# Performance work log

Hardware: AMD Instinct MI355X
Metric: run time of the kernel (lower is better)

## Reference

```python
import jax, jax.numpy as jnp
import numpy as np

N = 50000
E = 800000
NFEAT, NHID, NCLASS = 128, 128, 40


def setup_inputs() -> dict:
    key = jax.random.key(0)
    ks = jax.random.split(key, 8)
    x = jax.random.normal(ks[0], (N, NFEAT), dtype=jnp.float32)
    edge_index = jax.random.randint(ks[1], (2, E), 0, N, dtype=jnp.int64)
    def glorot(k, fan_in, fan_out):
        s = jnp.sqrt(6.0 / (fan_in + fan_out)).astype(jnp.float32)
        return jax.random.uniform(k, (fan_in, fan_out), jnp.float32, -s, s)
    W1 = glorot(ks[2], NFEAT, NHID); b1 = jnp.zeros((NHID,), jnp.float32)
    W2 = glorot(ks[3], NHID, NHID);  b2 = jnp.zeros((NHID,), jnp.float32)
    W3 = glorot(ks[4], NHID, NCLASS); b3 = jnp.zeros((NCLASS,), jnp.float32)
    return {"x": x, "edge_index": edge_index,
            "W1": W1, "b1": b1, "W2": W2, "b2": b2, "W3": W3, "b3": b3}


def _gcn_norm(edge_index, num_nodes, dtype):
    # Add self-loops, then symmetric normalization D^-1/2 (A+I) D^-1/2 (PyG gcn_norm).
    loop = jnp.arange(num_nodes, dtype=edge_index.dtype)
    src = jnp.concatenate([edge_index[0], loop])
    dst = jnp.concatenate([edge_index[1], loop])
    deg = jax.ops.segment_sum(jnp.ones_like(src, dtype=dtype), dst, num_segments=num_nodes)
    dinv = jnp.where(deg > 0, deg ** -0.5, 0.0).astype(dtype)
    norm = dinv[src] * dinv[dst]  # [E+N]
    return src, dst, norm


def _gcn_conv(h, src, dst, norm, W, b, num_nodes):
    h = h @ W                              # dense transform first (out_dim small)
    msg = h[src] * norm[:, None]           # gather + per-edge scale
    out = jax.ops.segment_sum(msg, dst, num_segments=num_nodes)  # scatter-add
    return out + b


def reference(x, edge_index, W1, b1, W2, b2, W3, b3):
    src, dst, norm = _gcn_norm(edge_index, N, x.dtype)
    h = jax.nn.relu(_gcn_conv(x, src, dst, norm, W1, b1, N))  # dropout: eval mode (identity)
    h = jax.nn.relu(_gcn_conv(h, src, dst, norm, W2, b2, N))
    h = _gcn_conv(h, src, dst, norm, W3, b3, N)
    return jax.nn.log_softmax(h, axis=-1)
```

## Files before the change

### kernel.cpp

```cpp
#include <hip/hip_runtime.h>
#include <stdint.h>

#define NN 50000
#define NE 800000
#define GG 782
#define NB 196
#define TT 8192
#define TB 98

typedef __attribute__((ext_vector_type(8))) short bfx8;
typedef __attribute__((ext_vector_type(4))) float f32x4;

__device__ inline unsigned short f2bf(float f) {
    union { float f; uint32_t u; } x; x.f = f;
    uint32_t u = x.u;
    return (unsigned short)((u + 0x7fffu + ((u >> 16) & 1u)) >> 16);
}
__device__ inline uint32_t pack2bf(float lo, float hi) {
    return (uint32_t)f2bf(lo) | ((uint32_t)f2bf(hi) << 16);
}
__device__ inline float bf2f(unsigned short h) {
    union { uint32_t u; float f; } c; c.u = ((uint32_t)h) << 16;
    return c.f;
}
__device__ inline float2 bfp2f2(uint32_t v) {
    union { uint32_t u; float f; } a, b;
    a.u = (v & 0xffffu) << 16;
    b.u = v & 0xffff0000u;
    return make_float2(a.f, b.f);
}
__device__ inline bfx8 ld8(const unsigned short* p) {
    union { uint4 u; bfx8 v; } c;
    c.u = *(const uint4*)p;
    return c.v;
}
__device__ inline bfx8 cvt8(float4 u, float4 v) {
    union { unsigned short s[8]; bfx8 r; } c;
    c.s[0] = f2bf(u.x); c.s[1] = f2bf(u.y); c.s[2] = f2bf(u.z); c.s[3] = f2bf(u.w);
    c.s[4] = f2bf(v.x); c.s[5] = f2bf(v.y); c.s[6] = f2bf(v.z); c.s[7] = f2bf(v.w);
    return c.r;
}

__global__ void prep(const float* __restrict__ W1, const float* __restrict__ W2,
                     const float* __restrict__ W3,
                     unsigned short* __restrict__ WT1, unsigned short* __restrict__ WT2,
                     unsigned short* __restrict__ WT3) {
    int w = blockIdx.x * 256 + threadIdx.x;
    if (w < 16384) {
        int nn = w >> 7, k = w & 127;
        WT1[nn * 128 + k] = f2bf(W1[k * 128 + nn]);
    } else if (w < 32768) {
        int w2 = w - 16384, nn = w2 >> 7, k = w2 & 127;
        WT2[nn * 128 + k] = f2bf(W2[k * 128 + nn]);
    } else if (w < 38912) {
        int w2 = w - 32768, nn = w2 >> 7, k = w2 & 127;
        WT3[nn * 128 + k] = (nn < 40) ? f2bf(W3[k * 40 + nn]) : (unsigned short)0;
    }
}

__global__ __launch_bounds__(256) void gemm1_hist(const float* __restrict__ X,
                                                  const unsigned short* __restrict__ WT,
                                                  unsigned short* __restrict__ G, int n,
                                                  const int* __restrict__ dst,
                                                  int* __restrict__ counts, int e) {
    if (blockIdx.x >= GG) {
        int b = blockIdx.x - GG;
        __shared__ int h[256];
        h[threadIdx.x] = 0;
        __syncthreads();
        int start = b * TT;
        int end = start + TT; if (end > e) end = e;
        for (int i = start + threadIdx.x; i < end; i += 256)
            atomicAdd(&h[dst[i] >> 8], 1);
        __syncthreads();
        int d = threadIdx.x;
        if (d < NB) counts[d * TB + b] = h[d];
        return;
    }
    int wave = threadIdx.x >> 6;
    int lane = threadIdx.x & 63;
    int quad = lane >> 4;
    int c = lane & 15;
    int rowbase = blockIdx.x * 64 + wave * 16;

    int arow = rowbase + c;
    if (arow >= n) arow = n - 1;
    const float* ap = X + (size_t)arow * 128 + quad * 8;
    bfx8 a[4];
#pragma unroll
    for (int kc = 0; kc < 4; kc++) {
        float4 u = *(const float4*)(ap + kc * 32);
        float4 v = *(const float4*)(ap + kc * 32 + 4);
        a[kc] = cvt8(u, v);
    }

    f32x4 acc[8];
#pragma unroll
    for (int ct = 0; ct < 8; ct++) acc[ct] = (f32x4){0.f, 0.f, 0.f, 0.f};
#pragma unroll
    for (int ct = 0; ct < 8; ct++) {
        const unsigned short* bp = WT + (size_t)(ct * 16 + c) * 128 + quad * 8;
#pragma unroll
        for (int kc = 0; kc < 4; kc++) {
            bfx8 b = ld8(bp + kc * 32);
            acc[ct] = __builtin_amdgcn_mfma_f32_16x16x32_bf16(a[kc], b, acc[ct], 0, 0, 0);
        }
    }

    int r0 = rowbase + quad * 4;
    bool odd = lane & 1;
#pragma unroll
    for (int ct = 0; ct < 8; ct++) {
        float x0 = acc[ct][0], x1 = acc[ct][1], x2 = acc[ct][2], x3 = acc[ct][3];
        float y0 = __shfl_xor(x0, 1, 64), y1 = __shfl_xor(x1, 1, 64);
        float y2 = __shfl_xor(x2, 1, 64), y3 = __shfl_xor(x3, 1, 64);
        int colp = ct * 16 + (c & ~1);
        if (!odd) {
            if (r0 + 0 < n) *(uint32_t*)(&G[(size_t)(r0 + 0) * 128 + colp]) = pack2bf(x0, y0);
            if (r0 + 1 < n) *(uint32_t*)(&G[(size_t)(r0 + 1) * 128 + colp]) = pack2bf(x1, y1);
        } else {
            if (r0 + 2 < n) *(uint32_t*)(&G[(size_t)(r0 + 2) * 128 + colp]) = pack2bf(y2, x2);
            if (r0 + 3 < n) *(uint32_t*)(&G[(size_t)(r0 + 3) * 128 + colp]) = pack2bf(y3, x3);
        }
    }
}

__global__ void scanA(int* __restrict__ counts, int* __restrict__ base196) {
    __shared__ int s[256];
    int d = threadIdx.x;
    int run = 0;
    if (d < NB) {
        for (int b0 = 0; b0 < TB; b0 += 14) {
            int c[14];
#pragma unroll
            for (int j = 0; j < 14; j++) {
                int b = b0 + j;
                c[j] = (b < TB) ? counts[d * TB + b] : 0;
            }
#pragma unroll
            for (int j = 0; j < 14; j++) {
                int b = b0 + j;
                if (b < TB) counts[d * TB + b] = run;
                run += c[j];
            }
        }
    }
    int v = run;
    s[d] = v;
    __syncthreads();
#pragma unroll
    for (int off = 1; off < 256; off <<= 1) {
        int y = (d >= off) ? s[d - off] : 0;
        __syncthreads();
        s[d] += y;
        __syncthreads();
    }
    if (d <= NB) base196[d] = s[d] - v;
}

__global__ __launch_bounds__(256) void scatterA(const int* __restrict__ src,
                                                const int* __restrict__ dst,
                                                const int* __restrict__ counts,
                                                const int* __restrict__ base196,
                                                uint32_t* __restrict__ packA, int e) {
    __shared__ int gb[256];
    __shared__ int lc[256];
    int t = threadIdx.x;
    if (t < NB) {
        gb[t] = base196[t] + counts[t * TB + blockIdx.x];
        lc[t] = 0;
    }
    __syncthreads();
    int start = blockIdx.x * TT;
    int end = start + TT; if (end > e) end = e;
    for (int i = start + t; i < end; i += 256) {
        int d = dst[i];
        int s = src[i];
        int hi = d >> 8;
        int r = atomicAdd(&lc[hi], 1);
        packA[gb[hi] + r] = ((uint32_t)d << 16) | (uint32_t)s;
    }
}

__global__ __launch_bounds__(256) void buildB(const uint32_t* __restrict__ packA,
                                              const int* __restrict__ base196,
                                              int* __restrict__ row_ptr, int* __restrict__ deg,
                                              float* __restrict__ dinv,
                                              unsigned short* __restrict__ csr_src, int n) {
    __shared__ int cnt[256];
    __shared__ int s[256];
    __shared__ int rp[256];
    int hi = blockIdx.x;
    int t = threadIdx.x;
    cnt[t] = 0;
    __syncthreads();
    int b0 = base196[hi], b1 = base196[hi + 1];
    for (int i = b0 + t; i < b1; i += 256)
        atomicAdd(&cnt[(packA[i] >> 16) & 0xFF], 1);
    __syncthreads();
    int v = cnt[t];
    s[t] = v;
    __syncthreads();
#pragma unroll
    for (int off = 1; off < 256; off <<= 1) {
        int y = (t >= off) ? s[t - off] : 0;
        __syncthreads();
        s[t] += y;
        __syncthreads();
    }
    rp[t] = b0 + s[t] - v;
    int node = hi * 256 + t;
    if (node < n) {
        row_ptr[node] = rp[t];
        deg[node] = v;
        dinv[node] = rsqrtf(1.0f + (float)v);
    }
    cnt[t] = 0;
    __syncthreads();
    for (int i = b0 + t; i < b1; i += 256) {
        uint32_t p = packA[i];
        int lo = (p >> 16) & 0xFF;
        int r = atomicAdd(&cnt[lo], 1);
        csr_src[rp[lo] + r] = (unsigned short)(p & 0xFFFF);
    }
}

__global__ __launch_bounds__(256) void gemm128_mfma(const unsigned short* __restrict__ A,
                                                    const unsigned short* __restrict__ WT,
                                                    const float* __restrict__ dinv,
                                                    unsigned short* __restrict__ G, int n) {
    int wave = threadIdx.x >> 6;
    int lane = threadIdx.x & 63;
    int quad = lane >> 4;
    int c = lane & 15;
    int rowbase = blockIdx.x * 64 + wave * 16;

    int arow = rowbase + c;
    if (arow >= n) arow = n - 1;
    const unsigned short* ap = A + (size_t)arow * 128 + quad * 8;
    bfx8 a[4];
#pragma unroll
    for (int kc = 0; kc < 4; kc++) a[kc] = ld8(ap + kc * 32);

    f32x4 acc[8];
#pragma unroll
    for (int ct = 0; ct < 8; ct++) acc[ct] = (f32x4){0.f, 0.f, 0.f, 0.f};
#pragma unroll
    for (int ct = 0; ct < 8; ct++) {
        const unsigned short* bp = WT + (size_t)(ct * 16 + c) * 128 + quad * 8;
#pragma unroll
        for (int kc = 0; kc < 4; kc++) {
            bfx8 b = ld8(bp + kc * 32);
            acc[ct] = __builtin_amdgcn_mfma_f32_16x16x32_bf16(a[kc], b, acc[ct], 0, 0, 0);
        }
    }

    int r0 = rowbase + quad * 4;
    float di[4];
#pragma unroll
    for (int r = 0; r < 4; r++) {
        int rr = r0 + r;
        di[r] = dinv[rr < n ? rr : 0];
    }
    bool odd = lane & 1;
#pragma unroll
    for (int ct = 0; ct < 8; ct++) {
        float x0 = acc[ct][0], x1 = acc[ct][1], x2 = acc[ct][2], x3 = acc[ct][3];
        float y0 = __shfl_xor(x0, 1, 64), y1 = __shfl_xor(x1, 1, 64);
        float y2 = __shfl_xor(x2, 1, 64), y3 = __shfl_xor(x3, 1, 64);
        int colp = ct * 16 + (c & ~1);
        if (!odd) {
            if (r0 + 0 < n) *(uint32_t*)(&G[(size_t)(r0 + 0) * 128 + colp]) = pack2bf(di[0] * x0, di[0] * y0);
            if (r0 + 1 < n) *(uint32_t*)(&G[(size_t)(r0 + 1) * 128 + colp]) = pack2bf(di[1] * x1, di[1] * y1);
        } else {
            if (r0 + 2 < n) *(uint32_t*)(&G[(size_t)(r0 + 2) * 128 + colp]) = pack2bf(di[2] * y2, di[2] * x2);
            if (r0 + 3 < n) *(uint32_t*)(&G[(size_t)(r0 + 3) * 128 + colp]) = pack2bf(di[3] * y3, di[3] * x3);
        }
    }
}

__global__ __launch_bounds__(256) void gemm40_mfma(const unsigned short* __restrict__ A,
                                                   const unsigned short* __restrict__ WT,
                                                   const float* __restrict__ dinv,
                                                   unsigned short* __restrict__ G, int n) {
    int wave = threadIdx.x >> 6;
    int lane = threadIdx.x & 63;
    int quad = lane >> 4;
    int c = lane & 15;
    int rowbase = blockIdx.x * 64 + wave * 16;

    int arow = rowbase + c;
    if (arow >= n) arow = n - 1;
    const unsigned short* ap = A + (size_t)arow * 128 + quad * 8;
    bfx8 a[4];
#pragma unroll
    for (int kc = 0; kc < 4; kc++) a[kc] = ld8(ap + kc * 32);

    f32x4 acc[3];
#pragma unroll
    for (int ct = 0; ct < 3; ct++) acc[ct] = (f32x4){0.f, 0.f, 0.f, 0.f};
#pragma unroll
    for (int ct = 0; ct < 3; ct++) {
        const unsigned short* bp = WT + (size_t)(ct * 16 + c) * 128 + quad * 8;
#pragma unroll
        for (int kc = 0; kc < 4; kc++) {
            bfx8 b = ld8(bp + kc * 32);
            acc[ct] = __builtin_amdgcn_mfma_f32_16x16x32_bf16(a[kc], b, acc[ct], 0, 0, 0);
        }
    }

    int r0 = rowbase + quad * 4;
    float di[4];
#pragma unroll
    for (int r = 0; r < 4; r++) {
        int rr = r0 + r;
        di[r] = dinv[rr < n ? rr : 0];
    }
    bool odd = lane & 1;
#pragma unroll
    for (int ct = 0; ct < 3; ct++) {
        float x0 = acc[ct][0], x1 = acc[ct][1], x2 = acc[ct][2], x3 = acc[ct][3];
        float y0 = __shfl_xor(x0, 1, 64), y1 = __shfl_xor(x1, 1, 64);
        float y2 = __shfl_xor(x2, 1, 64), y3 = __shfl_xor(x3, 1, 64);
        int colp = ct * 16 + (c & ~1);
        if (colp >= 40) continue;
        if (!odd) {
            if (r0 + 0 < n) *(uint32_t*)(&G[(size_t)(r0 + 0) * 40 + colp]) = pack2bf(di[0] * x0, di[0] * y0);
            if (r0 + 1 < n) *(uint32_t*)(&G[(size_t)(r0 + 1) * 40 + colp]) = pack2bf(di[1] * x1, di[1] * y1);
        } else {
            if (r0 + 2 < n) *(uint32_t*)(&G[(size_t)(r0 + 2) * 40 + colp]) = pack2bf(di[2] * y2, di[2] * x2);
            if (r0 + 3 < n) *(uint32_t*)(&G[(size_t)(r0 + 3) * 40 + colp]) = pack2bf(di[3] * y3, di[3] * x3);
        }
    }
}

__global__ __launch_bounds__(256) void agg128_l1(const unsigned short* __restrict__ G,
                                                 const int* __restrict__ row_ptr,
                                                 const int* __restrict__ deg,
                                                 const unsigned short* __restrict__ csr_src,
                                                 const float* __restrict__ dinv,
                                                 const float* __restrict__ b,
                                                 unsigned short* __restrict__ Y, int n) {
    int node = blockIdx.x * 4 + (threadIdx.x >> 6);
    if (node >= n) return;
    int l = threadIdx.x & 63;
    const uint32_t* Gr = (const uint32_t*)G;

    float dn = dinv[node];
    float2 sf = bfp2f2(Gr[(size_t)node * 64 + l]);
    float2 acc = make_float2(dn * sf.x, dn * sf.y);
    int p = row_ptr[node];
    int p1 = p + deg[node];
    for (; p + 7 < p1; p += 8) {
        int s0 = csr_src[p],     s1 = csr_src[p + 1], s2 = csr_src[p + 2], s3 = csr_src[p + 3];
        int s4 = csr_src[p + 4], s5 = csr_src[p + 5], s6 = csr_src[p + 6], s7 = csr_src[p + 7];
        float d0 = dinv[s0], d1 = dinv[s1], d2 = dinv[s2], d3 = dinv[s3];
        float d4 = dinv[s4], d5 = dinv[s5], d6 = dinv[s6], d7 = dinv[s7];
        float2 f0 = bfp2f2(Gr[(size_t)s0 * 64 + l]), f1 = bfp2f2(Gr[(size_t)s1 * 64 + l]);
        float2 f2 = bfp2f2(Gr[(size_t)s2 * 64 + l]), f3 = bfp2f2(Gr[(size_t)s3 * 64 + l]);
        float2 f4 = bfp2f2(Gr[(size_t)s4 * 64 + l]), f5 = bfp2f2(Gr[(size_t)s5 * 64 + l]);
        float2 f6 = bfp2f2(Gr[(size_t)s6 * 64 + l]), f7 = bfp2f2(Gr[(size_t)s7 * 64 + l]);
        acc.x += (fmaf(d0, f0.x, d1 * f1.x) + fmaf(d2, f2.x, d3 * f3.x)) +
                 (fmaf(d4, f4.x, d5 * f5.x) + fmaf(d6, f6.x, d7 * f7.x));
        acc.y += (fmaf(d0, f0.y, d1 * f1.y) + fmaf(d2, f2.y, d3 * f3.y)) +
                 (fmaf(d4, f4.y, d5 * f5.y) + fmaf(d6, f6.y, d7 * f7.y));
    }
    for (; p < p1; ++p) {
        int s = csr_src[p];
        float ds = dinv[s];
        float2 f = bfp2f2(Gr[(size_t)s * 64 + l]);
        acc.x = fmaf(ds, f.x, acc.x);
        acc.y = fmaf(ds, f.y, acc.y);
    }
    float vx = fmaf(dn, acc.x, b[2 * l]);
    float vy = fmaf(dn, acc.y, b[2 * l + 1]);
    ((uint32_t*)Y)[(size_t)node * 64 + l] = pack2bf(vx > 0.f ? vx : 0.f, vy > 0.f ? vy : 0.f);
}

__global__ __launch_bounds__(256) void agg128(const unsigned short* __restrict__ G,
                                              const int* __restrict__ row_ptr,
                                              const int* __restrict__ deg,
                                              const unsigned short* __restrict__ csr_src,
                                              const float* __restrict__ dinv,
                                              const float* __restrict__ b,
                                              unsigned short* __restrict__ Y, int n) {
    int node = blockIdx.x * 4 + (threadIdx.x >> 6);
    if (node >= n) return;
    int l = threadIdx.x & 63;
    const uint32_t* Gr = (const uint32_t*)G;

    float2 acc = bfp2f2(Gr[(size_t)node * 64 + l]);
    int p = row_ptr[node];
    int p1 = p + deg[node];
    for (; p + 7 < p1; p += 8) {
        int s0 = csr_src[p],     s1 = csr_src[p + 1], s2 = csr_src[p + 2], s3 = csr_src[p + 3];
        int s4 = csr_src[p + 4], s5 = csr_src[p + 5], s6 = csr_src[p + 6], s7 = csr_src[p + 7];
        float2 f0 = bfp2f2(Gr[(size_t)s0 * 64 + l]), f1 = bfp2f2(Gr[(size_t)s1 * 64 + l]);
        float2 f2 = bfp2f2(Gr[(size_t)s2 * 64 + l]), f3 = bfp2f2(Gr[(size_t)s3 * 64 + l]);
        float2 f4 = bfp2f2(Gr[(size_t)s4 * 64 + l]), f5 = bfp2f2(Gr[(size_t)s5 * 64 + l]);
        float2 f6 = bfp2f2(Gr[(size_t)s6 * 64 + l]), f7 = bfp2f2(Gr[(size_t)s7 * 64 + l]);
        acc.x += ((f0.x + f1.x) + (f2.x + f3.x)) + ((f4.x + f5.x) + (f6.x + f7.x));
        acc.y += ((f0.y + f1.y) + (f2.y + f3.y)) + ((f4.y + f5.y) + (f6.y + f7.y));
    }
    for (; p < p1; ++p) {
        float2 f = bfp2f2(Gr[(size_t)csr_src[p] * 64 + l]);
        acc.x += f.x; acc.y += f.y;
    }
    float dn = dinv[node];
    float vx = fmaf(dn, acc.x, b[2 * l]);
    float vy = fmaf(dn, acc.y, b[2 * l + 1]);
    ((uint32_t*)Y)[(size_t)node * 64 + l] = pack2bf(vx > 0.f ? vx : 0.f, vy > 0.f ? vy : 0.f);
}

__global__ __launch_bounds__(256) void agg40_lsm(const unsigned short* __restrict__ G,
                                                 const int* __restrict__ row_ptr,
                                                 const int* __restrict__ deg,
                                                 const unsigned short* __restrict__ csr_src,
                                                 const float* __restrict__ dinv,
                                                 const float* __restrict__ b,
                                                 float* __restrict__ Y, int n) {
    int node = blockIdx.x * 4 + (threadIdx.x >> 6);
    if (node >= n) return;
    int lane = threadIdx.x & 63;
    bool act = lane < 40;
    int lc = act ? lane : 0;

    float acc = act ? bf2f(G[(size_t)node * 40 + lane]) : 0.f;
    int p = row_ptr[node];
    int p1 = p + deg[node];
    for (; p + 3 < p1; p += 4) {
        int s0 = csr_src[p], s1 = csr_src[p + 1], s2 = csr_src[p + 2], s3 = csr_src[p + 3];
        float f0 = bf2f(G[(size_t)s0 * 40 + lc]);
        float f1 = bf2f(G[(size_t)s1 * 40 + lc]);
        float f2 = bf2f(G[(size_t)s2 * 40 + lc]);
        float f3 = bf2f(G[(size_t)s3 * 40 + lc]);
        acc += (f0 + f1) + (f2 + f3);
    }
    for (; p < p1; ++p) acc += bf2f(G[(size_t)csr_src[p] * 40 + lc]);

    float v = act ? fmaf(dinv[node], acc, b[lane]) : -1e30f;
    float m = v;
#pragma unroll
    for (int off = 32; off > 0; off >>= 1) m = fmaxf(m, __shfl_xor(m, off, 64));
    float ex = act ? expf(v - m) : 0.f;
    float s_ = ex;
#pragma unroll
    for (int off = 32; off > 0; off >>= 1) s_ += __shfl_xor(s_, off, 64);
    float ls = logf(s_);
    if (act) Y[(size_t)node * 40 + lane] = v - m - ls;
}


extern "C" void kernel_launch(void* const* d_in, const int* in_sizes, int n_in,
                              void* d_out, int out_size, void* d_ws, size_t ws_size,
                              hipStream_t stream) {
    const float* x  = (const float*)d_in[0];
    const int*   ei = (const int*)d_in[1];
    const float* W1 = (const float*)d_in[2];
    const float* b1 = (const float*)d_in[3];
    const float* W2 = (const float*)d_in[4];
    const float* b2 = (const float*)d_in[5];
    const float* W3 = (const float*)d_in[6];
    const float* b3 = (const float*)d_in[7];
    float* out = (float*)d_out;

    const int n = NN, e = NE;
    const int* srcI = ei;
    const int* dstI = ei + e;

    char* ws = (char*)d_ws;
    int*            deg     = (int*)ws;
    int*            row_ptr = (int*)(ws + 200704);
    float*          dinv    = (float*)(ws + 401408);
    int*            base196 = (int*)(ws + 602112);
    int*            counts  = (int*)(ws + 603136);
    uint32_t*       packA   = (uint32_t*)(ws + 681984);
    unsigned short* csr_src = (unsigned short*)(ws + 3881984);
    unsigned short* WT1     = (unsigned short*)(ws + 5481984);
    unsigned short* WT2     = (unsigned short*)(ws + 5514752);
    unsigned short* WT3     = (unsigned short*)(ws + 5547520);
    unsigned short* bufG    = (unsigned short*)(ws + 5559808);
    unsigned short* bufA    = (unsigned short*)(ws + 18359808);

    prep<<<152, 256, 0, stream>>>(W1, W2, W3, WT1, WT2, WT3);
    gemm1_hist<<<GG + TB, 256, 0, stream>>>(x, WT1, bufG, n, dstI, counts, e);
    scanA<<<1, 256, 0, stream>>>(counts, base196);
    scatterA<<<TB, 256, 0, stream>>>(srcI, dstI, counts, base196, packA, e);
    buildB<<<NB, 256, 0, stream>>>(packA, base196, row_ptr, deg, dinv, csr_src, n);
    agg128_l1<<<(n + 3) / 4, 256, 0, stream>>>(bufG, row_ptr, deg, csr_src, dinv, b1, bufA, n);
    gemm128_mfma<<<GG, 256, 0, stream>>>(bufA, WT2, dinv, bufG, n);
    agg128<<<(n + 3) / 4, 256, 0, stream>>>(bufG, row_ptr, deg, csr_src, dinv, b2, bufA, n);
    gemm40_mfma<<<GG, 256, 0, stream>>>(bufA, WT3, dinv, bufG, n);
    agg40_lsm<<<(n + 3) / 4, 256, 0, stream>>>(bufG, row_ptr, deg, csr_src, dinv, b3, out, n);
}
```

Measured before the change: 290.7 us.

## Replace count-scan-scatter CSR build with atomic-cursor bucketed slabs

Removes the separate scan and scatter kernels by having the histogram blocks in gemm1_hist claim per-bucket offsets with a global atomic cursor and write packed edges directly into fixed-size per-bucket slabs. buildB then computes bucket bases with an in-block prefix scan over the cursors. This cuts two kernel launches and one pass over the edge list. The cost is a larger workspace and nondeterministic ordering within buckets, and a bucket that holds more than SLAB edges would overflow.

After: 273.8 us. 1.06x faster.

```diff
diff --git a/kernel.cpp b/kernel.cpp
--- a/kernel.cpp
+++ b/kernel.cpp
@@ -5,8 +5,9 @@
 #define NE 800000
 #define GG 782
 #define NB 196
-#define TT 8192
-#define TB 98
+#define TT 2048
+#define SB 391
+#define SLAB 8192
 
 typedef __attribute__((ext_vector_type(8))) short bfx8;
 typedef __attribute__((ext_vector_type(4))) float f32x4;
@@ -44,7 +45,11 @@
 __global__ void prep(const float* __restrict__ W1, const float* __restrict__ W2,
                      const float* __restrict__ W3,
                      unsigned short* __restrict__ WT1, unsigned short* __restrict__ WT2,
-                     unsigned short* __restrict__ WT3) {
+                     unsigned short* __restrict__ WT3, int* __restrict__ cursor) {
+    if (blockIdx.x == 152) {
+        if (threadIdx.x < NB) cursor[threadIdx.x] = 0;
+        return;
+    }
     int w = blockIdx.x * 256 + threadIdx.x;
     if (w < 16384) {
         int nn = w >> 7, k = w & 127;
@@ -61,20 +66,42 @@
 __global__ __launch_bounds__(256) void gemm1_hist(const float* __restrict__ X,
                                                   const unsigned short* __restrict__ WT,
                                                   unsigned short* __restrict__ G, int n,
+                                                  const int* __restrict__ src,
                                                   const int* __restrict__ dst,
-                                                  int* __restrict__ counts, int e) {
+                                                  int* __restrict__ cursor,
+                                                  uint32_t* __restrict__ packA, int e) {
+    __shared__ int lc[NB];
+    __shared__ int gb[NB];
     if (blockIdx.x >= GG) {
         int b = blockIdx.x - GG;
-        __shared__ int h[256];
-        h[threadIdx.x] = 0;
+        int t = threadIdx.x;
+        if (t < NB) lc[t] = 0;
         __syncthreads();
         int start = b * TT;
         int end = start + TT; if (end > e) end = e;
-        for (int i = start + threadIdx.x; i < end; i += 256)
-            atomicAdd(&h[dst[i] >> 8], 1);
-        __syncthreads();
-        int d = threadIdx.x;
-        if (d < NB) counts[d * TB + b] = h[d];
+        int hi_[8], r_[8];
+        uint32_t pk_[8];
+#pragma unroll
+        for (int j = 0; j < 8; j++) {
+            int i = start + j * 256 + t;
+            if (i < end) {
+                int dd = dst[i], ss = src[i];
+                hi_[j] = dd >> 8;
+                pk_[j] = ((uint32_t)dd << 16) | (uint32_t)ss;
+                r_[j] = atomicAdd(&lc[hi_[j]], 1);
+            } else r_[j] = -1;
+        }
+        __syncthreads();
+        if (t < NB) {
+            int c = lc[t];
+            gb[t] = c ? atomicAdd(&cursor[t], c) : 0;
+        }
+        __syncthreads();
+#pragma unroll
+        for (int j = 0; j < 8; j++) {
+            if (r_[j] >= 0)
+                packA[(size_t)hi_[j] * SLAB + gb[hi_[j]] + r_[j]] = pk_[j];
+        }
         return;
     }
     int wave = threadIdx.x >> 6;
@@ -125,78 +152,35 @@
     }
 }
 
-__global__ void scanA(int* __restrict__ counts, int* __restrict__ base196) {
-    __shared__ int s[256];
-    int d = threadIdx.x;
-    int run = 0;
-    if (d < NB) {
-        for (int b0 = 0; b0 < TB; b0 += 14) {
-            int c[14];
-#pragma unroll
-            for (int j = 0; j < 14; j++) {
-                int b = b0 + j;
-                c[j] = (b < TB) ? counts[d * TB + b] : 0;
-            }
-#pragma unroll
-            for (int j = 0; j < 14; j++) {
-                int b = b0 + j;
-                if (b < TB) counts[d * TB + b] = run;
-                run += c[j];
-            }
-        }
-    }
-    int v = run;
-    s[d] = v;
-    __syncthreads();
-#pragma unroll
-    for (int off = 1; off < 256; off <<= 1) {
-        int y = (d >= off) ? s[d - off] : 0;
-        __syncthreads();
-        s[d] += y;
-        __syncthreads();
-    }
-    if (d <= NB) base196[d] = s[d] - v;
-}
-
-__global__ __launch_bounds__(256) void scatterA(const int* __restrict__ src,
-                                                const int* __restrict__ dst,
-                                                const int* __restrict__ counts,
-                                                const int* __restrict__ base196,
-                                                uint32_t* __restrict__ packA, int e) {
-    __shared__ int gb[256];
-    __shared__ int lc[256];
-    int t = threadIdx.x;
-    if (t < NB) {
-        gb[t] = base196[t] + counts[t * TB + blockIdx.x];
-        lc[t] = 0;
-    }
-    __syncthreads();
-    int start = blockIdx.x * TT;
-    int end = start + TT; if (end > e) end = e;
-    for (int i = start + t; i < end; i += 256) {
-        int d = dst[i];
-        int s = src[i];
-        int hi = d >> 8;
-        int r = atomicAdd(&lc[hi], 1);
-        packA[gb[hi] + r] = ((uint32_t)d << 16) | (uint32_t)s;
-    }
-}
-
 __global__ __launch_bounds__(256) void buildB(const uint32_t* __restrict__ packA,
-                                              const int* __restrict__ base196,
+                                              const int* __restrict__ cursor,
                                               int* __restrict__ row_ptr, int* __restrict__ deg,
                                               float* __restrict__ dinv,
                                               unsigned short* __restrict__ csr_src, int n) {
+    __shared__ int s[256];
     __shared__ int cnt[256];
-    __shared__ int s[256];
     __shared__ int rp[256];
+    __shared__ int basehi, bcnt;
     int hi = blockIdx.x;
     int t = threadIdx.x;
+    int bc = (t < NB) ? cursor[t] : 0;
+    s[t] = bc;
+    __syncthreads();
+#pragma unroll
+    for (int off = 1; off < 256; off <<= 1) {
+        int y = (t >= off) ? s[t - off] : 0;
+        __syncthreads();
+        s[t] += y;
+        __syncthreads();
+    }
+    if (t == hi) { basehi = s[t] - bc; bcnt = bc; }
     cnt[t] = 0;
     __syncthreads();
-    int b0 = base196[hi], b1 = base196[hi + 1];
-    for (int i = b0 + t; i < b1; i += 256)
-        atomicAdd(&cnt[(packA[i] >> 16) & 0xFF], 1);
+    int b0 = basehi;
+    int mc = bcnt;
+    const uint32_t* slab = packA + (size_t)hi * SLAB;
+    for (int i = t; i < mc; i += 256)
+        atomicAdd(&cnt[(slab[i] >> 16) & 0xFF], 1);
     __syncthreads();
     int v = cnt[t];
     s[t] = v;
@@ -217,8 +201,8 @@
     }
     cnt[t] = 0;
     __syncthreads();
-    for (int i = b0 + t; i < b1; i += 256) {
-        uint32_t p = packA[i];
+    for (int i = t; i < mc; i += 256) {
+        uint32_t p = slab[i];
         int lo = (p >> 16) & 0xFF;
         int r = atomicAdd(&cnt[lo], 1);
         csr_src[rp[lo] + r] = (unsigned short)(p & 0xFFFF);
@@ -472,21 +456,18 @@
     int*            deg     = (int*)ws;
     int*            row_ptr = (int*)(ws + 200704);
     float*          dinv    = (float*)(ws + 401408);
-    int*            base196 = (int*)(ws + 602112);
-    int*            counts  = (int*)(ws + 603136);
-    uint32_t*       packA   = (uint32_t*)(ws + 681984);
-    unsigned short* csr_src = (unsigned short*)(ws + 3881984);
-    unsigned short* WT1     = (unsigned short*)(ws + 5481984);
-    unsigned short* WT2     = (unsigned short*)(ws + 5514752);
-    unsigned short* WT3     = (unsigned short*)(ws + 5547520);
-    unsigned short* bufG    = (unsigned short*)(ws + 5559808);
-    unsigned short* bufA    = (unsigned short*)(ws + 18359808);
-
-    prep<<<152, 256, 0, stream>>>(W1, W2, W3, WT1, WT2, WT3);
-    gemm1_hist<<<GG + TB, 256, 0, stream>>>(x, WT1, bufG, n, dstI, counts, e);
-    scanA<<<1, 256, 0, stream>>>(counts, base196);
-    scatterA<<<TB, 256, 0, stream>>>(srcI, dstI, counts, base196, packA, e);
-    buildB<<<NB, 256, 0, stream>>>(packA, base196, row_ptr, deg, dinv, csr_src, n);
+    int*            cursor  = (int*)(ws + 602112);
+    uint32_t*       packA   = (uint32_t*)(ws + 603136);
+    unsigned short* csr_src = (unsigned short*)(ws + 7025664);
+    unsigned short* WT1     = (unsigned short*)(ws + 8625664);
+    unsigned short* WT2     = (unsigned short*)(ws + 8658432);
+    unsigned short* WT3     = (unsigned short*)(ws + 8691200);
+    unsigned short* bufG    = (unsigned short*)(ws + 8703488);
+    unsigned short* bufA    = (unsigned short*)(ws + 21503488);
+
+    prep<<<153, 256, 0, stream>>>(W1, W2, W3, WT1, WT2, WT3, cursor);
+    gemm1_hist<<<GG + SB, 256, 0, stream>>>(x, WT1, bufG, n, srcI, dstI, cursor, packA, e);
+    buildB<<<NB, 256, 0, stream>>>(packA, cursor, row_ptr, deg, dinv, csr_src, n);
     agg128_l1<<<(n + 3) / 4, 256, 0, stream>>>(bufG, row_ptr, deg, csr_src, dinv, b1, bufA, n);
     gemm128_mfma<<<GG, 256, 0, stream>>>(bufA, WT2, dinv, bufG, n);
     agg128<<<(n + 3) / 4, 256, 0, stream>>>(bufG, row_ptr, deg, csr_src, dinv, b2, bufA, n);
```
